# Optimization experiments

Hardware: AMD Instinct MI355X
Metric: run time of the kernel (lower is better)

Reference implementation:

```python
import jax, jax.numpy as jnp
import numpy as np

ROPE_THETA = 10000.0


def _rotate_half(x):
    # interleaved rotation: out[..., 2i] = -x[..., 2i+1], out[..., 2i+1] = x[..., 2i]
    x_even = x[..., ::2]
    x_odd = x[..., 1::2]
    return jnp.stack([-x_odd, x_even], axis=-1).reshape(x.shape)


def _rope_cos_sin(N, D, dtype):
    inv_freq = 1.0 / (ROPE_THETA ** (jnp.arange(0, D, 2, dtype=jnp.float32) / D))  # [D/2]
    angles = jnp.arange(N, dtype=jnp.float32)[:, None] * inv_freq[None, :]          # [N, D/2]
    angles = jnp.repeat(angles, 2, axis=-1)                                          # [N, D]
    cos = jnp.cos(angles).astype(dtype)[None, :, None, :]  # [1, N, 1, D]
    sin = jnp.sin(angles).astype(dtype)[None, :, None, :]
    return cos, sin


def setup_inputs() -> dict:
    key = jax.random.key(0)
    kq, kk, kv, km = jax.random.split(key, 4)
    B, N, H, D = 16, 1024, 8, 64
    xq = jax.random.normal(kq, (B, N, H, D), dtype=jnp.float32)
    xk = jax.random.normal(kk, (B, N, H, D), dtype=jnp.float32)
    xv = jax.random.normal(kv, (B, N, H, D), dtype=jnp.float32)
    vis_mask = jax.random.bernoulli(km, 0.8, (B, N))  # bool visibility mask per batch
    return {"xq": xq, "xk": xk, "xv": xv, "vis_mask": vis_mask}


def reference(xq, xk, xv, vis_mask):
    B, N, H, D = xq.shape
    sm_scale = 1.0 / np.sqrt(D).astype(np.float32)

    # RoPE (interleaved) on q and k
    cos, sin = _rope_cos_sin(N, D, xq.dtype)
    q = xq * cos + _rotate_half(xq) * sin
    k = xk * cos + _rotate_half(xk) * sin

    # masked full attention: scores [B, H, N, N]
    scores = jnp.einsum("bnhd,bmhd->bhnm", q, k) * sm_scale
    attn_mask = (vis_mask[:, None, :, None] & vis_mask[:, None, None, :])  # [B,1,N,N]
    scores = jnp.where(attn_mask, scores, -jnp.inf)
    p = jax.nn.softmax(scores, axis=-1)
    p = jnp.nan_to_num(p, nan=0.0)  # fully-masked rows -> zeros (matches fallback)
    out = jnp.einsum("bhnm,bmhd->bnhd", p, xv)
    return out
```

## Files before the change

### kernel.cpp

```cpp
#include <hip/hip_runtime.h>
#include <hip/hip_bf16.h>
#include <stdint.h>

#define Bb 16
#define Nn 1024
#define Hh 8
#define Dd 64

typedef unsigned short u16;
typedef float f32x4 __attribute__((ext_vector_type(4)));
typedef short short8 __attribute__((ext_vector_type(8)));

union U4S8 { uint4 u; short8 s; };
union BF2U { __hip_bfloat162 h; uint32_t u; };

__device__ __forceinline__ uint32_t f2bf(float f){
  union{float f;uint32_t i;} v; v.f=f;
  return (v.i + 0x7fffu + ((v.i>>16)&1u))>>16;
}

__device__ __forceinline__ f32x4 mfma16(short8 a, short8 b, f32x4 c){
  return __builtin_amdgcn_mfma_f32_16x16x32_bf16(a,b,c,0,0,0);
}

typedef __attribute__((address_space(3))) uint32_t lds_u32;
typedef const __attribute__((address_space(1))) uint32_t glb_u32;
__device__ __forceinline__ void gl_lds16(const u16* g, u16* l){
  __builtin_amdgcn_global_load_lds((glb_u32*)g, (lds_u32*)l, 16, 0, 0);
}

#define ROPE_K 0.41524101186092030f
#define QS 0.18033688011112042f
#define NEGBIG -1.0e30f

__global__ __launch_bounds__(256) void rope_table_kernel(float2* __restrict__ tab)
{
  int id = blockIdx.x*256 + threadIdx.x;
  int i = id >> 10, n = id & 1023;
  float inv = exp2f(-(float)i * ROPE_K);
  float sn, cs; sincosf((float)n * inv, &sn, &cs);
  tab[id] = make_float2(cs, sn);
}

template<int USE_TAB>
__global__ __launch_bounds__(256) void prepass_kernel(
    const float* __restrict__ xk, const float* __restrict__ xv,
    u16* __restrict__ Kf, u16* __restrict__ Vf,
    const float2* __restrict__ tab)
{
  const int tid = threadIdx.x;
  const int bid = blockIdx.x;
  const int nt = bid & 15, h = (bid>>4)&7, b = bid>>7;
  const size_t bh = (size_t)b*Hh + h;
  const size_t tile = (bh<<4) + nt;

  {
    int r = tid>>2, c = (tid&3)<<4;
    int n = (nt<<6) + r;
    const float4* g = (const float4*)(xk + ((((size_t)b*Nn + n)*Hh + h)<<6) + c);
    float4 a0=g[0],a1=g[1],a2=g[2],a3=g[3];
    float xx[16] = {a0.x,a0.y,a0.z,a0.w, a1.x,a1.y,a1.z,a1.w,
                    a2.x,a2.y,a2.z,a2.w, a3.x,a3.y,a3.z,a3.w};
    uint32_t w[8];
    #pragma unroll
    for (int j=0;j<8;++j){
      int ii = (c>>1)+j;
      float cs, sn;
      if (USE_TAB){
        float2 t = tab[(ii<<10)+n]; cs = t.x; sn = t.y;
      } else {
        float inv = exp2f(-(float)ii * ROPE_K);
        sincosf((float)n * inv, &sn, &cs);
      }
      float x0 = xx[2*j], x1 = xx[2*j+1];
      float q0 = x0*cs - x1*sn;
      float q1 = x1*cs + x0*sn;
      w[j] = f2bf(q0) | (f2bf(q1)<<16);
    }
    int kb = r>>4, l15 = r&15;
    int half = c>>5, qd = (c>>3)&3;
    u16* base = Kf + (tile<<12);
    int dest0 = (kb<<10) + (half<<9) + (qd<<7) + (l15<<3);
    *(uint4*)(base + dest0)       = make_uint4(w[0],w[1],w[2],w[3]);
    *(uint4*)(base + dest0 + 128) = make_uint4(w[4],w[5],w[6],w[7]);
  }

  {
    int k = tid&63, ds = (tid>>6)<<4;
    int n = (nt<<6) + k;
    int slot = (k&1) | (((k>>4)&3)<<1) | (((k>>2)&3)<<3) | (((k>>1)&1)<<5);
    int half = slot>>5, qd = (slot>>3)&3, j = slot&7;
    const float4* g = (const float4*)(xv + ((((size_t)b*Nn + n)*Hh + h)<<6) + ds);
    float4 a0=g[0],a1=g[1],a2=g[2],a3=g[3];
    float vv[16] = {a0.x,a0.y,a0.z,a0.w, a1.x,a1.y,a1.z,a1.w,
                    a2.x,a2.y,a2.z,a2.w, a3.x,a3.y,a3.z,a3.w};
    u16* base = Vf + (tile<<12);
    #pragma unroll
    for (int jj=0;jj<16;++jj){
      int d = ds + jj;
      int s = d>>4, l15v = d&15;
      base[(s<<10) + (half<<9) + (qd<<7) + (l15v<<3) + j] = (u16)f2bf(vv[jj]);
    }
  }
}

template<int USE_TAB>
__global__ __launch_bounds__(256,4) void attn8_kernel(
    const float* __restrict__ xq, const u16* __restrict__ Kf,
    const u16* __restrict__ Vf, const int* __restrict__ vis,
    const float2* __restrict__ tab, float* __restrict__ out)
{
  __shared__ u16 KV[2][2][4096];
  __shared__ float biasS[Nn];

  const int tid  = threadIdx.x;
  const int lane = tid & 63;
  const int wave = tid >> 6;
  const int l15  = lane & 15;
  const int quad = lane >> 4;

  const int bid = blockIdx.x;
  const int xcd = bid & 7;
  const int ix  = bid >> 3;
  const int bh_ = (xcd<<4) | (ix>>3);
  const int qt  = ix & 7;
  const int h   = bh_ & 7;
  const int b   = bh_ >> 3;
  const size_t bh = (size_t)bh_;
  const int qbase = qt<<7;

  const int* visb = vis + b*Nn;
  const u16* Kfb = Kf + (bh<<16);
  const u16* Vfb = Vf + (bh<<16);

  {
    int4 vi = *(const int4*)&visb[tid<<2];
    float4 bs;
    bs.x = vi.x ? 0.f : NEGBIG;
    bs.y = vi.y ? 0.f : NEGBIG;
    bs.z = vi.z ? 0.f : NEGBIG;
    bs.w = vi.w ? 0.f : NEGBIG;
    *(float4*)&biasS[tid<<2] = bs;
  }

  short8 qa[2][2];
  #pragma unroll
  for (int mb=0; mb<2; ++mb){
    int n = qbase + (wave<<5) + (mb<<4) + l15;
    const float* src = xq + ((((size_t)b*Nn + n)*Hh + h)<<6);
    #pragma unroll
    for (int half=0; half<2; ++half){
      int d0 = (half<<5) + (quad<<3);
      const float4* g = (const float4*)(src + d0);
      float4 u0 = g[0], u1 = g[1];
      float xx[8] = {u0.x,u0.y,u0.z,u0.w, u1.x,u1.y,u1.z,u1.w};
      uint32_t w[4];
      #pragma unroll
      for (int j=0;j<4;++j){
        int i2 = (d0>>1) + j;
        float cs, sn;
        if (USE_TAB){
          float2 t = tab[(i2<<10)+n]; cs = t.x; sn = t.y;
        } else {
          float inv = exp2f(-(float)i2 * ROPE_K);
          sincosf((float)n * inv, &sn, &cs);
        }
        float x0 = xx[2*j], x1 = xx[2*j+1];
        float q0 = (x0*cs - x1*sn)*QS;
        float q1 = (x1*cs + x0*sn)*QS;
        w[j] = f2bf(q0) | (f2bf(q1)<<16);
      }
      U4S8 t; t.u = make_uint4(w[0],w[1],w[2],w[3]);
      qa[mb][half] = t.s;
    }
  }

  U4S8 ones_u; ones_u.u = make_uint4(0x3F803F80u,0x3F803F80u,0x3F803F80u,0x3F803F80u);
  const short8 ones = ones_u.s;

  f32x4 acc[2][4];
  f32x4 l_acc[2];
  #pragma unroll
  for (int mb=0;mb<2;++mb){
    l_acc[mb] = (f32x4){0.f,0.f,0.f,0.f};
    #pragma unroll
    for (int s=0;s<4;++s) acc[mb][s] = (f32x4){0.f,0.f,0.f,0.f};
  }

  const int t8 = tid<<3;

  gl_lds16(Kfb + t8,        &KV[0][0][t8]);
  gl_lds16(Kfb + 2048 + t8, &KV[0][0][2048 + t8]);
  gl_lds16(Vfb + t8,        &KV[0][1][t8]);
  gl_lds16(Vfb + 2048 + t8, &KV[0][1][2048 + t8]);
  __syncthreads();

  for (int kt=0; kt<16; ++kt){
    const int cur = kt & 1;
    if (kt < 15){
      const u16* kg = Kfb + ((kt+1)<<12);
      const u16* vg = Vfb + ((kt+1)<<12);
      gl_lds16(kg + t8,        &KV[cur^1][0][t8]);
      gl_lds16(kg + 2048 + t8, &KV[cur^1][0][2048 + t8]);
      gl_lds16(vg + t8,        &KV[cur^1][1][t8]);
      gl_lds16(vg + 2048 + t8, &KV[cur^1][1][2048 + t8]);
    }

    uint32_t pk[4][2][2];
    #pragma unroll
    for (int kb=0;kb<4;++kb){
      short8 kf0 = *(const short8*)&KV[cur][0][(kb<<10) + (lane<<3)];
      short8 kf1 = *(const short8*)&KV[cur][0][(kb<<10) + 512 + (lane<<3)];
      f32x4 bias = *(const f32x4*)&biasS[(kt<<6)+(kb<<4)+(quad<<2)];
      #pragma unroll
      for (int mb=0;mb<2;++mb){
        f32x4 t = mfma16(kf0, qa[mb][0], bias);
        t = mfma16(kf1, qa[mb][1], t);
        float p0 = __builtin_amdgcn_exp2f(t.x);
        float p1 = __builtin_amdgcn_exp2f(t.y);
        float p2 = __builtin_amdgcn_exp2f(t.z);
        float p3 = __builtin_amdgcn_exp2f(t.w);
        BF2U e0; e0.h = __float22bfloat162_rn(make_float2(p0,p1));
        BF2U e1; e1.h = __float22bfloat162_rn(make_float2(p2,p3));
        pk[kb][0][mb] = e0.u;
        pk[kb][1][mb] = e1.u;
      }
    }

    short8 pa[2][2];
    #pragma unroll
    for (int mb=0;mb<2;++mb){
      U4S8 a0; a0.u = make_uint4(pk[0][0][mb], pk[1][0][mb], pk[2][0][mb], pk[3][0][mb]);
      U4S8 a1; a1.u = make_uint4(pk[0][1][mb], pk[1][1][mb], pk[2][1][mb], pk[3][1][mb]);
      pa[mb][0] = a0.s; pa[mb][1] = a1.s;
    }

    #pragma unroll
    for (int mb=0;mb<2;++mb){
      l_acc[mb] = mfma16(pa[mb][0], ones, l_acc[mb]);
      l_acc[mb] = mfma16(pa[mb][1], ones, l_acc[mb]);
    }
    #pragma unroll
    for (int s=0;s<4;++s){
      short8 vb0 = *(const short8*)&KV[cur][1][(s<<10) + (lane<<3)];
      short8 vb1 = *(const short8*)&KV[cur][1][(s<<10) + 512 + (lane<<3)];
      #pragma unroll
      for (int mb=0;mb<2;++mb){
        acc[mb][s] = mfma16(pa[mb][0], vb0, acc[mb][s]);
        acc[mb][s] = mfma16(pa[mb][1], vb1, acc[mb][s]);
      }
    }

    __syncthreads();
  }

  #pragma unroll
  for (int mb=0;mb<2;++mb){
    #pragma unroll
    for (int rr=0;rr<4;++rr){
      int qrow = qbase + (wave<<5) + (mb<<4) + (quad<<2) + rr;
      float lq = l_acc[mb][rr];
      float invl = (biasS[qrow] == 0.f && lq > 0.f) ? 1.f/lq : 0.f;
      float* ob = out + ((((size_t)b*Nn + qrow)*Hh + h)<<6);
      #pragma unroll
      for (int s=0;s<4;++s)
        ob[(s<<4)+l15] = acc[mb][s][rr]*invl;
    }
  }
}

__device__ __forceinline__ void stage_rope_row_fb(const float* __restrict__ src,
                                                  u16 (*dst)[72],
                                                  int n_global, int sr, int d0)
{
  const float4* g = (const float4*)src;
  float4 a0 = g[0], a1 = g[1], a2 = g[2], a3 = g[3];
  float xx[16] = {a0.x,a0.y,a0.z,a0.w, a1.x,a1.y,a1.z,a1.w,
                  a2.x,a2.y,a2.z,a2.w, a3.x,a3.y,a3.z,a3.w};
  uint32_t w[8];
  #pragma unroll
  for (int j=0;j<8;++j){
    int i = (d0>>1)+j;
    float inv = exp2f(-(float)i * ROPE_K);
    float ang = (float)n_global * inv;
    float sn, cs; sincosf(ang, &sn, &cs);
    float x0 = xx[2*j], x1 = xx[2*j+1];
    float q0 = x0*cs - x1*sn;
    float q1 = x1*cs + x0*sn;
    w[j] = f2bf(q0) | (f2bf(q1)<<16);
  }
  *(uint4*)&dst[sr][d0]   = make_uint4(w[0],w[1],w[2],w[3]);
  *(uint4*)&dst[sr][d0+8] = make_uint4(w[4],w[5],w[6],w[7]);
}

__global__ __launch_bounds__(256,2) void attn_fallback(
    const float* __restrict__ xq, const float* __restrict__ xk,
    const float* __restrict__ xv, const int* __restrict__ vis,
    float* __restrict__ out)
{
  __shared__ u16 Qs[64][72];
  __shared__ u16 Ks[64][72];
  __shared__ u16 Vt[64][72];
  __shared__ u16 Ps[4][16][72];
  __shared__ float viss[64];

  const int tid  = threadIdx.x;
  const int wave = tid >> 6;
  const int lane = tid & 63;
  const int l15  = lane & 15;
  const int quad = lane >> 4;

  const int bid = blockIdx.x;
  const int qt = bid & 15;
  const int h  = (bid >> 4) & 7;
  const int b  = bid >> 7;

  const int sr = tid >> 2;
  const int d0 = (tid & 3) << 4;

  {
    int ng = (qt<<6) + sr;
    const float* src = xq + ((((size_t)b*Nn + ng)*Hh + h)<<6) + d0;
    stage_rope_row_fb(src, Qs, ng, sr, d0);
  }
  __syncthreads();

  short8 qa0 = *(const short8*)&Qs[(wave<<4)+l15][quad<<3];
  short8 qa1 = *(const short8*)&Qs[(wave<<4)+l15][(quad<<3)+32];

  f32x4 acc[4];
  #pragma unroll
  for (int s=0;s<4;++s) acc[s] = (f32x4){0.f,0.f,0.f,0.f};
  float m_r[4], l_r[4];
  #pragma unroll
  for (int rr=0;rr<4;++rr){ m_r[rr] = -1e30f; l_r[rr] = 0.f; }

  for (int kt=0; kt<16; ++kt){
    __syncthreads();
    {
      int ng = (kt<<6) + sr;
      const float* src = xk + ((((size_t)b*Nn + ng)*Hh + h)<<6) + d0;
      stage_rope_row_fb(src, Ks, ng, sr, d0);
    }
    {
      int ng = (kt<<6) + sr;
      const float4* g = (const float4*)(xv + ((((size_t)b*Nn + ng)*Hh + h)<<6) + d0);
      float4 a0 = g[0], a1 = g[1], a2 = g[2], a3 = g[3];
      float vv16[16] = {a0.x,a0.y,a0.z,a0.w, a1.x,a1.y,a1.z,a1.w,
                        a2.x,a2.y,a2.z,a2.w, a3.x,a3.y,a3.z,a3.w};
      #pragma unroll
      for (int j=0;j<16;++j) Vt[d0+j][sr] = (u16)f2bf(vv16[j]);
    }
    if (tid < 64) viss[tid] = (vis[b*Nn + (kt<<6) + tid] != 0) ? 1.f : 0.f;
    __syncthreads();

    f32x4 s4[4];
    #pragma unroll
    for (int n=0;n<4;++n){
      short8 kb0 = *(const short8*)&Ks[(n<<4)+l15][quad<<3];
      short8 kb1 = *(const short8*)&Ks[(n<<4)+l15][(quad<<3)+32];
      f32x4 t = (f32x4){0.f,0.f,0.f,0.f};
      t = mfma16(qa0, kb0, t);
      t = mfma16(qa1, kb1, t);
      s4[n] = t;
    }
    float vv[4];
    #pragma unroll
    for (int n=0;n<4;++n) vv[n] = viss[(n<<4)+l15];

    float p[4][4];
    #pragma unroll
    for (int rr=0; rr<4; ++rr){
      float sc[4];
      #pragma unroll
      for (int n=0;n<4;++n) sc[n] = (vv[n] > 0.f) ? s4[n][rr]*0.125f : -1e30f;
      float tm = fmaxf(fmaxf(sc[0],sc[1]), fmaxf(sc[2],sc[3]));
      tm = fmaxf(tm, __shfl_xor(tm,1));
      tm = fmaxf(tm, __shfl_xor(tm,2));
      tm = fmaxf(tm, __shfl_xor(tm,4));
      tm = fmaxf(tm, __shfl_xor(tm,8));
      float mnew  = fmaxf(m_r[rr], tm);
      float alpha = __expf(m_r[rr] - mnew);
      m_r[rr] = mnew;
      float psum = 0.f;
      #pragma unroll
      for (int n=0;n<4;++n){
        float pv = (vv[n] > 0.f) ? __expf(sc[n] - mnew) : 0.f;
        p[n][rr] = pv; psum += pv;
      }
      l_r[rr] = l_r[rr]*alpha + psum;
      #pragma unroll
      for (int s=0;s<4;++s) acc[s][rr] *= alpha;
    }

    #pragma unroll
    for (int n=0;n<4;++n)
      #pragma unroll
      for (int rr=0;rr<4;++rr)
        Ps[wave][(quad<<2)+rr][(n<<4)+l15] = (u16)f2bf(p[n][rr]);
    asm volatile("s_waitcnt lgkmcnt(0)" ::: "memory");
    short8 pa0 = *(const short8*)&Ps[wave][l15][quad<<3];
    short8 pa1 = *(const short8*)&Ps[wave][l15][(quad<<3)+32];

    #pragma unroll
    for (int s=0;s<4;++s){
      short8 vb0 = *(const short8*)&Vt[(s<<4)+l15][quad<<3];
      short8 vb1 = *(const short8*)&Vt[(s<<4)+l15][(quad<<3)+32];
      acc[s] = mfma16(pa0, vb0, acc[s]);
      acc[s] = mfma16(pa1, vb1, acc[s]);
    }
  }

  #pragma unroll
  for (int rr=0;rr<4;++rr){
    float t = l_r[rr];
    t += __shfl_xor(t,1); t += __shfl_xor(t,2);
    t += __shfl_xor(t,4); t += __shfl_xor(t,8);
    int row = (qt<<6) + (wave<<4) + (quad<<2) + rr;
    int qv  = vis[b*Nn + row];
    float invl = (qv != 0 && t > 0.f) ? 1.f/t : 0.f;
    size_t obase = (((size_t)b*Nn + row)*Hh + h) << 6;
    #pragma unroll
    for (int s=0;s<4;++s)
      out[obase + (s<<4) + l15] = acc[s][rr]*invl;
  }
}

extern "C" void kernel_launch(void* const* d_in, const int* in_sizes, int n_in,
                              void* d_out, int out_size, void* d_ws, size_t ws_size,
                              hipStream_t stream)
{
  const float* xq = (const float*)d_in[0];
  const float* xk = (const float*)d_in[1];
  const float* xv = (const float*)d_in[2];
  const int* vis  = (const int*)d_in[3];
  float* out = (float*)d_out;

  const size_t kv_elems = (size_t)Bb*Hh*Nn*Dd;
  const size_t kv_bytes = kv_elems*sizeof(u16);
  const size_t need_kv  = 2*kv_bytes;
  const size_t tab_bytes = (size_t)32*1024*sizeof(float2);

  if (d_ws != nullptr && ws_size >= need_kv + tab_bytes){
    u16* Kf = (u16*)d_ws;
    u16* Vf = Kf + kv_elems;
    float2* tab = (float2*)((char*)d_ws + need_kv);
    rope_table_kernel<<<dim3(128), dim3(256), 0, stream>>>(tab);
    prepass_kernel<1><<<dim3(Bb*Hh*(Nn/64)), dim3(256), 0, stream>>>(xk, xv, Kf, Vf, tab);
    attn8_kernel<1><<<dim3(Bb*Hh*(Nn/128)), dim3(256), 0, stream>>>(xq, Kf, Vf, vis, tab, out);
  } else if (d_ws != nullptr && ws_size >= need_kv){
    u16* Kf = (u16*)d_ws;
    u16* Vf = Kf + kv_elems;
    prepass_kernel<0><<<dim3(Bb*Hh*(Nn/64)), dim3(256), 0, stream>>>(xk, xv, Kf, Vf, nullptr);
    attn8_kernel<0><<<dim3(Bb*Hh*(Nn/128)), dim3(256), 0, stream>>>(xq, Kf, Vf, vis, nullptr, out);
  } else {
    attn_fallback<<<dim3(Bb*Hh*(Nn/64)), dim3(256), 0, stream>>>(xq, xk, xv, vis, out);
  }
}
```

Before: 189.6 us.

## Fuse K/V RoPE and bf16 conversion prepass into the attention kernel

Removes the separate prepass that wrote rotated bf16 K and swizzled V to a workspace. The attention kernel now loads fp32 K/V straight from global memory, applies RoPE and converts to bf16 into registers, and writes the next tile into LDS after computing the current one. Blocks grow to 512 threads covering 256 query rows, the RoPE table is transposed to [n][i] so reads are contiguous, and setprio hints are placed around the MFMA sections. This drops the workspace round trip and one launch. In exchange, each of the 4 query-tile blocks per (b,h) repeats the K/V conversion, and the global loads are now synchronous register loads rather than async global-to-LDS copies.

```diff
diff --git a/kernel.cpp b/kernel.cpp
--- a/kernel.cpp
+++ b/kernel.cpp
@@ -23,12 +23,6 @@
   return __builtin_amdgcn_mfma_f32_16x16x32_bf16(a,b,c,0,0,0);
 }
 
-typedef __attribute__((address_space(3))) uint32_t lds_u32;
-typedef const __attribute__((address_space(1))) uint32_t glb_u32;
-__device__ __forceinline__ void gl_lds16(const u16* g, u16* l){
-  __builtin_amdgcn_global_load_lds((glb_u32*)g, (lds_u32*)l, 16, 0, 0);
-}
-
 #define ROPE_K 0.41524101186092030f
 #define QS 0.18033688011112042f
 #define NEGBIG -1.0e30f
@@ -36,78 +30,55 @@
 __global__ __launch_bounds__(256) void rope_table_kernel(float2* __restrict__ tab)
 {
   int id = blockIdx.x*256 + threadIdx.x;
-  int i = id >> 10, n = id & 1023;
+  int n = id >> 5, i = id & 31;
   float inv = exp2f(-(float)i * ROPE_K);
   float sn, cs; sincosf((float)n * inv, &sn, &cs);
   tab[id] = make_float2(cs, sn);
 }
 
-template<int USE_TAB>
-__global__ __launch_bounds__(256) void prepass_kernel(
+struct Stage {
+  float4 ka0, ka1, va0, va1, c0, c1;
+};
+
+__device__ __forceinline__ void stage_load(Stage& S,
     const float* __restrict__ xk, const float* __restrict__ xv,
-    u16* __restrict__ Kf, u16* __restrict__ Vf,
-    const float2* __restrict__ tab)
-{
-  const int tid = threadIdx.x;
-  const int bid = blockIdx.x;
-  const int nt = bid & 15, h = (bid>>4)&7, b = bid>>7;
-  const size_t bh = (size_t)b*Hh + h;
-  const size_t tile = (bh<<4) + nt;
-
-  {
-    int r = tid>>2, c = (tid&3)<<4;
-    int n = (nt<<6) + r;
-    const float4* g = (const float4*)(xk + ((((size_t)b*Nn + n)*Hh + h)<<6) + c);
-    float4 a0=g[0],a1=g[1],a2=g[2],a3=g[3];
-    float xx[16] = {a0.x,a0.y,a0.z,a0.w, a1.x,a1.y,a1.z,a1.w,
-                    a2.x,a2.y,a2.z,a2.w, a3.x,a3.y,a3.z,a3.w};
-    uint32_t w[8];
-    #pragma unroll
-    for (int j=0;j<8;++j){
-      int ii = (c>>1)+j;
-      float cs, sn;
-      if (USE_TAB){
-        float2 t = tab[(ii<<10)+n]; cs = t.x; sn = t.y;
-      } else {
-        float inv = exp2f(-(float)ii * ROPE_K);
-        sincosf((float)n * inv, &sn, &cs);
-      }
-      float x0 = xx[2*j], x1 = xx[2*j+1];
-      float q0 = x0*cs - x1*sn;
-      float q1 = x1*cs + x0*sn;
-      w[j] = f2bf(q0) | (f2bf(q1)<<16);
-    }
-    int kb = r>>4, l15 = r&15;
-    int half = c>>5, qd = (c>>3)&3;
-    u16* base = Kf + (tile<<12);
-    int dest0 = (kb<<10) + (half<<9) + (qd<<7) + (l15<<3);
-    *(uint4*)(base + dest0)       = make_uint4(w[0],w[1],w[2],w[3]);
-    *(uint4*)(base + dest0 + 128) = make_uint4(w[4],w[5],w[6],w[7]);
-  }
-
-  {
-    int k = tid&63, ds = (tid>>6)<<4;
-    int n = (nt<<6) + k;
-    int slot = (k&1) | (((k>>4)&3)<<1) | (((k>>2)&3)<<3) | (((k>>1)&1)<<5);
-    int half = slot>>5, qd = (slot>>3)&3, j = slot&7;
-    const float4* g = (const float4*)(xv + ((((size_t)b*Nn + n)*Hh + h)<<6) + ds);
-    float4 a0=g[0],a1=g[1],a2=g[2],a3=g[3];
-    float vv[16] = {a0.x,a0.y,a0.z,a0.w, a1.x,a1.y,a1.z,a1.w,
-                    a2.x,a2.y,a2.z,a2.w, a3.x,a3.y,a3.z,a3.w};
-    u16* base = Vf + (tile<<12);
-    #pragma unroll
-    for (int jj=0;jj<16;++jj){
-      int d = ds + jj;
-      int s = d>>4, l15v = d&15;
-      base[(s<<10) + (half<<9) + (qd<<7) + (l15v<<3) + j] = (u16)f2bf(vv[jj]);
-    }
-  }
-}
-
-template<int USE_TAB>
-__global__ __launch_bounds__(256,4) void attn8_kernel(
-    const float* __restrict__ xq, const u16* __restrict__ Kf,
-    const u16* __restrict__ Vf, const int* __restrict__ vis,
+    const float2* __restrict__ tab, int b, int h, int n, int sd0)
+{
+  const float4* kg = (const float4*)(xk + ((((size_t)b*Nn + n)*Hh + h)<<6) + sd0);
+  S.ka0 = kg[0]; S.ka1 = kg[1];
+  const float4* vg = (const float4*)(xv + ((((size_t)b*Nn + n)*Hh + h)<<6) + sd0);
+  S.va0 = vg[0]; S.va1 = vg[1];
+  const float4* tg = (const float4*)(tab + (n<<5) + (sd0>>1));
+  S.c0 = tg[0]; S.c1 = tg[1];
+}
+
+__device__ __forceinline__ void stage_write(const Stage& S,
+    u16* __restrict__ Kl, u16* __restrict__ Vl,
+    int kdest, int sd0, int vhalf, int vqd, int vj)
+{
+  float kx[8]  = {S.ka0.x,S.ka0.y,S.ka0.z,S.ka0.w, S.ka1.x,S.ka1.y,S.ka1.z,S.ka1.w};
+  float cs4[4] = {S.c0.x, S.c0.z, S.c1.x, S.c1.z};
+  float sn4[4] = {S.c0.y, S.c0.w, S.c1.y, S.c1.w};
+  uint32_t w[4];
+  #pragma unroll
+  for (int j=0;j<4;++j){
+    float x0 = kx[2*j], x1 = kx[2*j+1];
+    float q0 = x0*cs4[j] - x1*sn4[j];
+    float q1 = x1*cs4[j] + x0*sn4[j];
+    w[j] = f2bf(q0) | (f2bf(q1)<<16);
+  }
+  *(uint4*)&Kl[kdest] = make_uint4(w[0],w[1],w[2],w[3]);
+  float vvv[8] = {S.va0.x,S.va0.y,S.va0.z,S.va0.w, S.va1.x,S.va1.y,S.va1.z,S.va1.w};
+  #pragma unroll
+  for (int jj=0;jj<8;++jj){
+    int d = sd0 + jj;
+    Vl[((d>>4)<<10) + (vhalf<<9) + (vqd<<7) + ((d&15)<<3) + vj] = (u16)f2bf(vvv[jj]);
+  }
+}
+
+__global__ __launch_bounds__(512,4) void fused_attn_kernel(
+    const float* __restrict__ xq, const float* __restrict__ xk,
+    const float* __restrict__ xv, const int* __restrict__ vis,
     const float2* __restrict__ tab, float* __restrict__ out)
 {
   __shared__ u16 KV[2][2][4096];
@@ -122,25 +93,26 @@
   const int bid = blockIdx.x;
   const int xcd = bid & 7;
   const int ix  = bid >> 3;
-  const int bh_ = (xcd<<4) | (ix>>3);
-  const int qt  = ix & 7;
+  const int bh_ = (xcd<<4) | (ix>>2);
+  const int qt  = ix & 3;
   const int h   = bh_ & 7;
   const int b   = bh_ >> 3;
-  const size_t bh = (size_t)bh_;
-  const int qbase = qt<<7;
+  const int qbase = qt<<8;
 
   const int* visb = vis + b*Nn;
-  const u16* Kfb = Kf + (bh<<16);
-  const u16* Vfb = Vf + (bh<<16);
+
+  const int srow = tid >> 3;
+  const int sd0  = (tid & 7) << 3;
+  const int kdest = ((srow>>4)<<10) + ((sd0>>5)<<9) + (((sd0>>3)&3)<<7) + ((srow&15)<<3);
+  const int slot = (srow&1) | (((srow>>4)&3)<<1) | (((srow>>2)&3)<<3) | (((srow>>1)&1)<<5);
+  const int vhalf = slot>>5, vqd = (slot>>3)&3, vj = slot&7;
 
   {
-    int4 vi = *(const int4*)&visb[tid<<2];
-    float4 bs;
+    int2 vi = *(const int2*)&visb[tid<<1];
+    float2 bs;
     bs.x = vi.x ? 0.f : NEGBIG;
     bs.y = vi.y ? 0.f : NEGBIG;
-    bs.z = vi.z ? 0.f : NEGBIG;
-    bs.w = vi.w ? 0.f : NEGBIG;
-    *(float4*)&biasS[tid<<2] = bs;
+    *(float2*)&biasS[tid<<1] = bs;
   }
 
   short8 qa[2][2];
@@ -158,20 +130,14 @@
       #pragma unroll
       for (int j=0;j<4;++j){
         int i2 = (d0>>1) + j;
-        float cs, sn;
-        if (USE_TAB){
-          float2 t = tab[(i2<<10)+n]; cs = t.x; sn = t.y;
-        } else {
-          float inv = exp2f(-(float)i2 * ROPE_K);
-          sincosf((float)n * inv, &sn, &cs);
-        }
+        float2 t = tab[(n<<5)+i2];
         float x0 = xx[2*j], x1 = xx[2*j+1];
-        float q0 = (x0*cs - x1*sn)*QS;
-        float q1 = (x1*cs + x0*sn)*QS;
+        float q0 = (x0*t.x - x1*t.y)*QS;
+        float q1 = (x1*t.x + x0*t.y)*QS;
         w[j] = f2bf(q0) | (f2bf(q1)<<16);
       }
-      U4S8 t; t.u = make_uint4(w[0],w[1],w[2],w[3]);
-      qa[mb][half] = t.s;
+      U4S8 t2; t2.u = make_uint4(w[0],w[1],w[2],w[3]);
+      qa[mb][half] = t2.s;
     }
   }
 
@@ -187,26 +153,22 @@
     for (int s=0;s<4;++s) acc[mb][s] = (f32x4){0.f,0.f,0.f,0.f};
   }
 
-  const int t8 = tid<<3;
-
-  gl_lds16(Kfb + t8,        &KV[0][0][t8]);
-  gl_lds16(Kfb + 2048 + t8, &KV[0][0][2048 + t8]);
-  gl_lds16(Vfb + t8,        &KV[0][1][t8]);
-  gl_lds16(Vfb + 2048 + t8, &KV[0][1][2048 + t8]);
+  {
+    Stage S;
+    stage_load(S, xk, xv, tab, b, h, srow, sd0);
+    stage_write(S, &KV[0][0][0], &KV[0][1][0], kdest, sd0, vhalf, vqd, vj);
+  }
   __syncthreads();
 
   for (int kt=0; kt<16; ++kt){
     const int cur = kt & 1;
-    if (kt < 15){
-      const u16* kg = Kfb + ((kt+1)<<12);
-      const u16* vg = Vfb + ((kt+1)<<12);
-      gl_lds16(kg + t8,        &KV[cur^1][0][t8]);
-      gl_lds16(kg + 2048 + t8, &KV[cur^1][0][2048 + t8]);
-      gl_lds16(vg + t8,        &KV[cur^1][1][t8]);
-      gl_lds16(vg + 2048 + t8, &KV[cur^1][1][2048 + t8]);
-    }
+
+    Stage S;
+    if (kt < 15)
+      stage_load(S, xk, xv, tab, b, h, ((kt+1)<<6) + srow, sd0);
 
     uint32_t pk[4][2][2];
+    __builtin_amdgcn_s_setprio(1);
     #pragma unroll
     for (int kb=0;kb<4;++kb){
       short8 kf0 = *(const short8*)&KV[cur][0][(kb<<10) + (lane<<3)];
@@ -226,6 +188,7 @@
         pk[kb][1][mb] = e1.u;
       }
     }
+    __builtin_amdgcn_s_setprio(0);
 
     short8 pa[2][2];
     #pragma unroll
@@ -235,6 +198,7 @@
       pa[mb][0] = a0.s; pa[mb][1] = a1.s;
     }
 
+    __builtin_amdgcn_s_setprio(1);
     #pragma unroll
     for (int mb=0;mb<2;++mb){
       l_acc[mb] = mfma16(pa[mb][0], ones, l_acc[mb]);
@@ -250,6 +214,10 @@
         acc[mb][s] = mfma16(pa[mb][1], vb1, acc[mb][s]);
       }
     }
+    __builtin_amdgcn_s_setprio(0);
+
+    if (kt < 15)
+      stage_write(S, &KV[cur^1][0][0], &KV[cur^1][1][0], kdest, sd0, vhalf, vqd, vj);
 
     __syncthreads();
   }
@@ -436,23 +404,12 @@
   const int* vis  = (const int*)d_in[3];
   float* out = (float*)d_out;
 
-  const size_t kv_elems = (size_t)Bb*Hh*Nn*Dd;
-  const size_t kv_bytes = kv_elems*sizeof(u16);
-  const size_t need_kv  = 2*kv_bytes;
   const size_t tab_bytes = (size_t)32*1024*sizeof(float2);
 
-  if (d_ws != nullptr && ws_size >= need_kv + tab_bytes){
-    u16* Kf = (u16*)d_ws;
-    u16* Vf = Kf + kv_elems;
-    float2* tab = (float2*)((char*)d_ws + need_kv);
+  if (d_ws != nullptr && ws_size >= tab_bytes){
+    float2* tab = (float2*)d_ws;
     rope_table_kernel<<<dim3(128), dim3(256), 0, stream>>>(tab);
-    prepass_kernel<1><<<dim3(Bb*Hh*(Nn/64)), dim3(256), 0, stream>>>(xk, xv, Kf, Vf, tab);
-    attn8_kernel<1><<<dim3(Bb*Hh*(Nn/128)), dim3(256), 0, stream>>>(xq, Kf, Vf, vis, tab, out);
-  } else if (d_ws != nullptr && ws_size >= need_kv){
-    u16* Kf = (u16*)d_ws;
-    u16* Vf = Kf + kv_elems;
-    prepass_kernel<0><<<dim3(Bb*Hh*(Nn/64)), dim3(256), 0, stream>>>(xk, xv, Kf, Vf, nullptr);
-    attn8_kernel<0><<<dim3(Bb*Hh*(Nn/128)), dim3(256), 0, stream>>>(xq, Kf, Vf, vis, nullptr, out);
+    fused_attn_kernel<<<dim3(Bb*Hh*4), dim3(512), 0, stream>>>(xq, xk, xv, vis, tab, out);
   } else {
     attn_fallback<<<dim3(Bb*Hh*(Nn/64)), dim3(256), 0, stream>>>(xq, xk, xv, vis, out);
   }
```

Result: faster. 181.8 us (-4.1%).
